# Kernel tuning notes

Measured on AMD Instinct MI355X. Metric: run time of the kernel, lower is better.

## Reference

```python
import jax, jax.numpy as jnp
import numpy as np

SHAPE = (4096, 8192)


def setup_inputs() -> dict:
    key = jax.random.key(0)
    k1, k2 = jax.random.split(key)
    weights = jax.random.normal(k1, SHAPE, dtype=jnp.float32)
    mask_weights = jax.random.normal(k2, SHAPE, dtype=jnp.float32)
    return {
        "weights": weights,
        "mask_weights": mask_weights,
        "masking_percent_x100": 50,
    }


def reference(weights, mask_weights, masking_percent_x100):
    # Faithful to MaskingFunction.forward:
    #   k = int((1 - masking_percent) * N); zero the k SMALLEST mask_weights positions in weights.
    masking_percent = masking_percent_x100 / 100.0
    n = mask_weights.size  # static
    k = int((1.0 - masking_percent) * n)  # static Python int -> jit-compatible
    flat_mask = mask_weights.reshape(-1)
    # bottom-k == top-k of negated values
    _, bottomk_idx = jax.lax.top_k(-flat_mask, k)
    masked = weights.reshape(-1).at[bottomk_idx].set(0.0)
    return masked.reshape(weights.shape)
```

## Files before the change

kernel.cpp:

```cpp
#include <hip/hip_runtime.h>


#define NBINS 2048
#define CAP1 (1u << 22)
#define CAP2 65536u

__device__ unsigned long long g_k;
__device__ long long          g_b1;
__device__ unsigned long long g_rem1;
__device__ unsigned int       g_hist1[NBINS];
__device__ unsigned int       g_hist2[NBINS];
__device__ unsigned int       g_count1;
__device__ unsigned int       g_count2;
__device__ unsigned long long g_kstar_excl;
__device__ unsigned int       g_cand_u[CAP1];
__device__ unsigned int       g_cand_i[CAP1];
__device__ unsigned long long g_cand2[CAP2];

static __device__ __forceinline__ unsigned int xf(unsigned int b) {
  return b ^ ((unsigned int)((int)b >> 31) | 0x80000000u);
}

__global__ __launch_bounds__(256) void k_init(const int* __restrict__ mp, long long n) {
  int t = threadIdx.x;
  for (int i = t; i < NBINS; i += 256) { g_hist1[i] = 0; g_hist2[i] = 0; }
  if (t == 0) {
    long long m = (long long)(*mp);
    long long k = (n * (100 - m)) / 100;
    if (k < 0) k = 0;
    if (k > n) k = n;
    g_k = (unsigned long long)k;
    g_count1 = 0;
    g_count2 = 0;
    g_kstar_excl = 0;
    g_b1 = -1;
    g_rem1 = 0;
  }
}

__global__ __launch_bounds__(256) void hist1_kernel(const unsigned int* __restrict__ mb,
                                                    long long n4, long long n) {
  __shared__ unsigned int sh[4 * NBINS];
  const int t = threadIdx.x;
  for (int i = t; i < 4 * NBINS; i += 256) sh[i] = 0;
  __syncthreads();
  unsigned int* h = &sh[(t >> 6) * NBINS];
  const long long stride = (long long)gridDim.x * 256;
  const uint4* mb4 = (const uint4*)mb;
  for (long long i = (long long)blockIdx.x * 256 + t; i < n4; i += stride) {
    uint4 v = mb4[i];
    atomicAdd(&h[xf(v.x) >> 21], 1u);
    atomicAdd(&h[xf(v.y) >> 21], 1u);
    atomicAdd(&h[xf(v.z) >> 21], 1u);
    atomicAdd(&h[xf(v.w) >> 21], 1u);
  }
  if (blockIdx.x == 0) {
    long long rs = n4 << 2;
    if ((long long)t < n - rs) atomicAdd(&h[xf(mb[rs + t]) >> 21], 1u);
  }
  __syncthreads();
  for (int i = t; i < NBINS; i += 256) {
    unsigned int s = sh[i] + sh[i + NBINS] + sh[i + 2 * NBINS] + sh[i + 3 * NBINS];
    if (s) atomicAdd(&g_hist1[i], s);
  }
}

__global__ __launch_bounds__(256) void select1_kernel() {
  __shared__ unsigned long long tsum[256];
  __shared__ long long s_bin;
  __shared__ unsigned long long s_rem;
  const int t = threadIdx.x;
  unsigned long long k = g_k;
  if (k == 0) return;
  unsigned int local[8];
  unsigned long long s = 0;
#pragma unroll
  for (int j = 0; j < 8; j++) { local[j] = g_hist1[t * 8 + j]; s += local[j]; }
  tsum[t] = s;
  __syncthreads();
  for (int off = 1; off < 256; off <<= 1) {
    unsigned long long v = (t >= off) ? tsum[t - off] : 0ull;
    __syncthreads();
    tsum[t] += v;
    __syncthreads();
  }
  unsigned long long incl = tsum[t], excl = incl - s;
  if (excl < k && k <= incl) {
    unsigned long long cum = excl;
#pragma unroll
    for (int j = 0; j < 8; j++) {
      if (cum + local[j] >= k) { s_bin = t * 8 + j; s_rem = k - cum; break; }
      cum += local[j];
    }
  }
  __syncthreads();
  if (t == 0) { g_b1 = s_bin; g_rem1 = s_rem; }
}

__global__ __launch_bounds__(256) void pass2_kernel(const unsigned int* __restrict__ mb,
                                                    const float* __restrict__ w,
                                                    float* __restrict__ out,
                                                    long long n4, long long n) {
  __shared__ unsigned int sh2[NBINS];
  const int t = threadIdx.x;
  for (int i = t; i < NBINS; i += 256) sh2[i] = 0;
  __syncthreads();
  const long long b1 = g_b1;
  const long long stride = (long long)gridDim.x * 256;
  const uint4*  mb4 = (const uint4*)mb;
  const float4* w4  = (const float4*)w;
  float4*       o4  = (float4*)out;
  for (long long i = (long long)blockIdx.x * 256 + t; i < n4; i += stride) {
    uint4  mv = mb4[i];
    float4 wv = w4[i];
    unsigned int u0 = xf(mv.x), u1 = xf(mv.y), u2 = xf(mv.z), u3 = xf(mv.w);
    float4 o;
    o.x = ((long long)(u0 >> 21) < b1) ? 0.0f : wv.x;
    o.y = ((long long)(u1 >> 21) < b1) ? 0.0f : wv.y;
    o.z = ((long long)(u2 >> 21) < b1) ? 0.0f : wv.z;
    o.w = ((long long)(u3 >> 21) < b1) ? 0.0f : wv.w;
    o4[i] = o;
    long long base = i << 2;
    if ((long long)(u0 >> 21) == b1) {
      unsigned int s = atomicAdd(&g_count1, 1u);
      if (s < CAP1) { g_cand_u[s] = u0; g_cand_i[s] = (unsigned int)(base + 0); }
      atomicAdd(&sh2[(u0 >> 10) & (NBINS - 1)], 1u);
    }
    if ((long long)(u1 >> 21) == b1) {
      unsigned int s = atomicAdd(&g_count1, 1u);
      if (s < CAP1) { g_cand_u[s] = u1; g_cand_i[s] = (unsigned int)(base + 1); }
      atomicAdd(&sh2[(u1 >> 10) & (NBINS - 1)], 1u);
    }
    if ((long long)(u2 >> 21) == b1) {
      unsigned int s = atomicAdd(&g_count1, 1u);
      if (s < CAP1) { g_cand_u[s] = u2; g_cand_i[s] = (unsigned int)(base + 2); }
      atomicAdd(&sh2[(u2 >> 10) & (NBINS - 1)], 1u);
    }
    if ((long long)(u3 >> 21) == b1) {
      unsigned int s = atomicAdd(&g_count1, 1u);
      if (s < CAP1) { g_cand_u[s] = u3; g_cand_i[s] = (unsigned int)(base + 3); }
      atomicAdd(&sh2[(u3 >> 10) & (NBINS - 1)], 1u);
    }
  }
  if (blockIdx.x == 0) {
    long long rs = n4 << 2;
    long long i = rs + t;
    if (i < n) {
      unsigned int u = xf(mb[i]);
      out[i] = ((long long)(u >> 21) < b1) ? 0.0f : w[i];
      if ((long long)(u >> 21) == b1) {
        unsigned int s = atomicAdd(&g_count1, 1u);
        if (s < CAP1) { g_cand_u[s] = u; g_cand_i[s] = (unsigned int)i; }
        atomicAdd(&sh2[(u >> 10) & (NBINS - 1)], 1u);
      }
    }
  }
  __syncthreads();
  for (int i = t; i < NBINS; i += 256)
    if (sh2[i]) atomicAdd(&g_hist2[i], sh2[i]);
}

__global__ __launch_bounds__(256) void finalize_kernel() {
  __shared__ unsigned long long tsum[256];
  __shared__ long long s_b2;
  __shared__ unsigned long long s_rem2;
  const int t = threadIdx.x;
  long long b1 = g_b1;
  if (b1 < 0) return;
  {
    unsigned long long k = g_rem1;
    unsigned int local[8];
    unsigned long long s = 0;
#pragma unroll
    for (int j = 0; j < 8; j++) { local[j] = g_hist2[t * 8 + j]; s += local[j]; }
    tsum[t] = s;
    __syncthreads();
    for (int off = 1; off < 256; off <<= 1) {
      unsigned long long v = (t >= off) ? tsum[t - off] : 0ull;
      __syncthreads();
      tsum[t] += v;
      __syncthreads();
    }
    unsigned long long incl = tsum[t], excl = incl - s;
    if (excl < k && k <= incl) {
      unsigned long long cum = excl;
#pragma unroll
      for (int j = 0; j < 8; j++) {
        if (cum + local[j] >= k) { s_b2 = t * 8 + j; s_rem2 = k - cum; break; }
        cum += local[j];
      }
    }
    __syncthreads();
  }
  const unsigned int b2 = (unsigned int)s_b2;
  const unsigned int C = (g_count1 < CAP1) ? g_count1 : CAP1;
  for (unsigned int i = t; i < C; i += 256) {
    unsigned int u = g_cand_u[i];
    if (((u >> 10) & (NBINS - 1)) == b2) {
      unsigned int slot = atomicAdd(&g_count2, 1u);
      if (slot < CAP2) g_cand2[slot] = ((unsigned long long)u << 32) | (unsigned long long)g_cand_i[i];
    }
  }
  __threadfence();
  __syncthreads();
  unsigned int c2 = atomicAdd(&g_count2, 0u);
  const unsigned int C2 = (c2 < CAP2) ? c2 : CAP2;
  const unsigned long long rem2 = s_rem2;
  for (unsigned int i = t; i < C2; i += 256) {
    unsigned long long key = g_cand2[i];
    unsigned long long cnt = 0;
    for (unsigned int j = 0; j < C2; j++) cnt += (g_cand2[j] < key) ? 1ull : 0ull;
    if (cnt + 1 == rem2) g_kstar_excl = key + 1;
  }
}

__global__ __launch_bounds__(256) void fixup_kernel(float* __restrict__ out) {
  const unsigned long long kstar = g_kstar_excl;
  const unsigned int C = (g_count1 < CAP1) ? g_count1 : CAP1;
  const long long stride = (long long)gridDim.x * blockDim.x;
  for (long long i = (long long)blockIdx.x * blockDim.x + threadIdx.x; i < (long long)C; i += stride) {
    unsigned int idx = g_cand_i[i];
    unsigned long long key = ((unsigned long long)g_cand_u[i] << 32) | (unsigned long long)idx;
    if (key < kstar) out[idx] = 0.0f;
  }
}

extern "C" void kernel_launch(void* const* d_in, const int* in_sizes, int n_in,
                              void* d_out, int out_size, void* d_ws, size_t ws_size,
                              hipStream_t stream) {
  const float*        w  = (const float*)d_in[0];
  const unsigned int* mb = (const unsigned int*)d_in[1];
  const int*          mp = (const int*)d_in[2];
  float* out = (float*)d_out;
  const long long n  = (long long)in_sizes[0];
  const long long n4 = n >> 2;

  int blocks = (int)((n4 + 255) / 256);
  if (blocks > 2048) blocks = 2048;
  if (blocks < 1) blocks = 1;

  k_init<<<1, 256, 0, stream>>>(mp, n);
  hist1_kernel<<<blocks, 256, 0, stream>>>(mb, n4, n);
  select1_kernel<<<1, 256, 0, stream>>>();
  pass2_kernel<<<blocks, 256, 0, stream>>>(mb, w, out, n4, n);
  finalize_kernel<<<1, 256, 0, stream>>>();
  fixup_kernel<<<256, 256, 0, stream>>>(out);
}
```

Measured before the change: 368.3 us.

## Fuse select/init/fixup stages into fewer kernels and unroll streaming loops

Cuts the pipeline from six launches to three. The bin-select prefix scan is folded into every pass2 block. The init kernel is replaced by resetting the histograms and counters at the end of finalize, and the fixup scatter now runs inside the single-block finalize. The hist1 loop is unrolled to four uint4 loads per thread and the pass2 loop to two. The pass2 second-level histogram now uses global atomics directly instead of a shared histogram. The aim is to remove launch overhead and add memory-level parallelism, at the cost of redundant per-block scans and reliance on globals starting at zero on the first call.

```diff
diff --git a/kernel.cpp b/kernel.cpp
--- a/kernel.cpp
+++ b/kernel.cpp
@@ -5,14 +5,10 @@
 #define CAP1 (1u << 22)
 #define CAP2 65536u
 
-__device__ unsigned long long g_k;
-__device__ long long          g_b1;
-__device__ unsigned long long g_rem1;
 __device__ unsigned int       g_hist1[NBINS];
 __device__ unsigned int       g_hist2[NBINS];
 __device__ unsigned int       g_count1;
 __device__ unsigned int       g_count2;
-__device__ unsigned long long g_kstar_excl;
 __device__ unsigned int       g_cand_u[CAP1];
 __device__ unsigned int       g_cand_i[CAP1];
 __device__ unsigned long long g_cand2[CAP2];
@@ -21,21 +17,12 @@
   return b ^ ((unsigned int)((int)b >> 31) | 0x80000000u);
 }
 
-__global__ __launch_bounds__(256) void k_init(const int* __restrict__ mp, long long n) {
-  int t = threadIdx.x;
-  for (int i = t; i < NBINS; i += 256) { g_hist1[i] = 0; g_hist2[i] = 0; }
-  if (t == 0) {
-    long long m = (long long)(*mp);
-    long long k = (n * (100 - m)) / 100;
-    if (k < 0) k = 0;
-    if (k > n) k = n;
-    g_k = (unsigned long long)k;
-    g_count1 = 0;
-    g_count2 = 0;
-    g_kstar_excl = 0;
-    g_b1 = -1;
-    g_rem1 = 0;
-  }
+static __device__ __forceinline__ long long compute_k(const int* mp, long long n) {
+  long long m = (long long)(*mp);
+  long long k = (n * (100 - m)) / 100;
+  if (k < 0) k = 0;
+  if (k > n) k = n;
+  return k;
 }
 
 __global__ __launch_bounds__(256) void hist1_kernel(const unsigned int* __restrict__ mb,
@@ -45,14 +32,40 @@
   for (int i = t; i < 4 * NBINS; i += 256) sh[i] = 0;
   __syncthreads();
   unsigned int* h = &sh[(t >> 6) * NBINS];
-  const long long stride = (long long)gridDim.x * 256;
   const uint4* mb4 = (const uint4*)mb;
-  for (long long i = (long long)blockIdx.x * 256 + t; i < n4; i += stride) {
-    uint4 v = mb4[i];
-    atomicAdd(&h[xf(v.x) >> 21], 1u);
-    atomicAdd(&h[xf(v.y) >> 21], 1u);
-    atomicAdd(&h[xf(v.z) >> 21], 1u);
-    atomicAdd(&h[xf(v.w) >> 21], 1u);
+  const long long stride = (long long)gridDim.x * 1024;
+  long long i0 = (long long)blockIdx.x * 1024 + t;
+  for (; i0 + 768 < n4; i0 += stride) {
+    uint4 v0 = mb4[i0];
+    uint4 v1 = mb4[i0 + 256];
+    uint4 v2 = mb4[i0 + 512];
+    uint4 v3 = mb4[i0 + 768];
+    atomicAdd(&h[xf(v0.x) >> 21], 1u);
+    atomicAdd(&h[xf(v0.y) >> 21], 1u);
+    atomicAdd(&h[xf(v0.z) >> 21], 1u);
+    atomicAdd(&h[xf(v0.w) >> 21], 1u);
+    atomicAdd(&h[xf(v1.x) >> 21], 1u);
+    atomicAdd(&h[xf(v1.y) >> 21], 1u);
+    atomicAdd(&h[xf(v1.z) >> 21], 1u);
+    atomicAdd(&h[xf(v1.w) >> 21], 1u);
+    atomicAdd(&h[xf(v2.x) >> 21], 1u);
+    atomicAdd(&h[xf(v2.y) >> 21], 1u);
+    atomicAdd(&h[xf(v2.z) >> 21], 1u);
+    atomicAdd(&h[xf(v2.w) >> 21], 1u);
+    atomicAdd(&h[xf(v3.x) >> 21], 1u);
+    atomicAdd(&h[xf(v3.y) >> 21], 1u);
+    atomicAdd(&h[xf(v3.z) >> 21], 1u);
+    atomicAdd(&h[xf(v3.w) >> 21], 1u);
+  }
+  for (int g = 0; g < 3; ++g) {
+    long long i = i0 + (long long)g * 256;
+    if (i < n4) {
+      uint4 v = mb4[i];
+      atomicAdd(&h[xf(v.x) >> 21], 1u);
+      atomicAdd(&h[xf(v.y) >> 21], 1u);
+      atomicAdd(&h[xf(v.z) >> 21], 1u);
+      atomicAdd(&h[xf(v.w) >> 21], 1u);
+    }
   }
   if (blockIdx.x == 0) {
     long long rs = n4 << 2;
@@ -65,82 +78,82 @@
   }
 }
 
-__global__ __launch_bounds__(256) void select1_kernel() {
-  __shared__ unsigned long long tsum[256];
-  __shared__ long long s_bin;
-  __shared__ unsigned long long s_rem;
-  const int t = threadIdx.x;
-  unsigned long long k = g_k;
-  if (k == 0) return;
-  unsigned int local[8];
-  unsigned long long s = 0;
-#pragma unroll
-  for (int j = 0; j < 8; j++) { local[j] = g_hist1[t * 8 + j]; s += local[j]; }
-  tsum[t] = s;
-  __syncthreads();
-  for (int off = 1; off < 256; off <<= 1) {
-    unsigned long long v = (t >= off) ? tsum[t - off] : 0ull;
-    __syncthreads();
-    tsum[t] += v;
-    __syncthreads();
-  }
-  unsigned long long incl = tsum[t], excl = incl - s;
-  if (excl < k && k <= incl) {
-    unsigned long long cum = excl;
-#pragma unroll
-    for (int j = 0; j < 8; j++) {
-      if (cum + local[j] >= k) { s_bin = t * 8 + j; s_rem = k - cum; break; }
-      cum += local[j];
-    }
-  }
-  __syncthreads();
-  if (t == 0) { g_b1 = s_bin; g_rem1 = s_rem; }
+static __device__ __forceinline__ void cand_add(unsigned int u, unsigned int idx) {
+  unsigned int s = atomicAdd(&g_count1, 1u);
+  if (s < CAP1) { g_cand_u[s] = u; g_cand_i[s] = idx; }
+  atomicAdd(&g_hist2[(u >> 10) & (NBINS - 1)], 1u);
+}
+
+static __device__ __forceinline__ void proc4(long long i, uint4 mv, float4 wv,
+                                             float4* __restrict__ o4, long long b1) {
+  unsigned int u0 = xf(mv.x), u1 = xf(mv.y), u2 = xf(mv.z), u3 = xf(mv.w);
+  float4 o;
+  o.x = ((long long)(u0 >> 21) < b1) ? 0.0f : wv.x;
+  o.y = ((long long)(u1 >> 21) < b1) ? 0.0f : wv.y;
+  o.z = ((long long)(u2 >> 21) < b1) ? 0.0f : wv.z;
+  o.w = ((long long)(u3 >> 21) < b1) ? 0.0f : wv.w;
+  o4[i] = o;
+  long long base = i << 2;
+  if ((long long)(u0 >> 21) == b1) cand_add(u0, (unsigned int)(base + 0));
+  if ((long long)(u1 >> 21) == b1) cand_add(u1, (unsigned int)(base + 1));
+  if ((long long)(u2 >> 21) == b1) cand_add(u2, (unsigned int)(base + 2));
+  if ((long long)(u3 >> 21) == b1) cand_add(u3, (unsigned int)(base + 3));
 }
 
 __global__ __launch_bounds__(256) void pass2_kernel(const unsigned int* __restrict__ mb,
                                                     const float* __restrict__ w,
                                                     float* __restrict__ out,
+                                                    const int* __restrict__ mp,
                                                     long long n4, long long n) {
-  __shared__ unsigned int sh2[NBINS];
+  __shared__ unsigned long long tsum[256];
+  __shared__ long long s_b1;
   const int t = threadIdx.x;
-  for (int i = t; i < NBINS; i += 256) sh2[i] = 0;
-  __syncthreads();
-  const long long b1 = g_b1;
-  const long long stride = (long long)gridDim.x * 256;
+  if (t == 0) s_b1 = -1;
+  __syncthreads();
+  const unsigned long long k = (unsigned long long)compute_k(mp, n);
+  if (k != 0) {
+    unsigned int local[8];
+    unsigned long long s = 0;
+#pragma unroll
+    for (int j = 0; j < 8; j++) { local[j] = g_hist1[t * 8 + j]; s += local[j]; }
+    tsum[t] = s;
+    __syncthreads();
+    for (int off = 1; off < 256; off <<= 1) {
+      unsigned long long v = (t >= off) ? tsum[t - off] : 0ull;
+      __syncthreads();
+      tsum[t] += v;
+      __syncthreads();
+    }
+    unsigned long long incl = tsum[t], excl = incl - s;
+    if (excl < k && k <= incl) {
+      unsigned long long cum = excl;
+#pragma unroll
+      for (int j = 0; j < 8; j++) {
+        if (cum + local[j] >= k) { s_b1 = t * 8 + j; break; }
+        cum += local[j];
+      }
+    }
+  }
+  __syncthreads();
+  const long long b1 = s_b1;
+
   const uint4*  mb4 = (const uint4*)mb;
   const float4* w4  = (const float4*)w;
   float4*       o4  = (float4*)out;
-  for (long long i = (long long)blockIdx.x * 256 + t; i < n4; i += stride) {
-    uint4  mv = mb4[i];
-    float4 wv = w4[i];
-    unsigned int u0 = xf(mv.x), u1 = xf(mv.y), u2 = xf(mv.z), u3 = xf(mv.w);
-    float4 o;
-    o.x = ((long long)(u0 >> 21) < b1) ? 0.0f : wv.x;
-    o.y = ((long long)(u1 >> 21) < b1) ? 0.0f : wv.y;
-    o.z = ((long long)(u2 >> 21) < b1) ? 0.0f : wv.z;
-    o.w = ((long long)(u3 >> 21) < b1) ? 0.0f : wv.w;
-    o4[i] = o;
-    long long base = i << 2;
-    if ((long long)(u0 >> 21) == b1) {
-      unsigned int s = atomicAdd(&g_count1, 1u);
-      if (s < CAP1) { g_cand_u[s] = u0; g_cand_i[s] = (unsigned int)(base + 0); }
-      atomicAdd(&sh2[(u0 >> 10) & (NBINS - 1)], 1u);
-    }
-    if ((long long)(u1 >> 21) == b1) {
-      unsigned int s = atomicAdd(&g_count1, 1u);
-      if (s < CAP1) { g_cand_u[s] = u1; g_cand_i[s] = (unsigned int)(base + 1); }
-      atomicAdd(&sh2[(u1 >> 10) & (NBINS - 1)], 1u);
-    }
-    if ((long long)(u2 >> 21) == b1) {
-      unsigned int s = atomicAdd(&g_count1, 1u);
-      if (s < CAP1) { g_cand_u[s] = u2; g_cand_i[s] = (unsigned int)(base + 2); }
-      atomicAdd(&sh2[(u2 >> 10) & (NBINS - 1)], 1u);
-    }
-    if ((long long)(u3 >> 21) == b1) {
-      unsigned int s = atomicAdd(&g_count1, 1u);
-      if (s < CAP1) { g_cand_u[s] = u3; g_cand_i[s] = (unsigned int)(base + 3); }
-      atomicAdd(&sh2[(u3 >> 10) & (NBINS - 1)], 1u);
-    }
+  const long long stride = (long long)gridDim.x * 512;
+  long long i0 = (long long)blockIdx.x * 512 + t;
+  for (; i0 + 256 < n4; i0 += stride) {
+    uint4  mv0 = mb4[i0];
+    uint4  mv1 = mb4[i0 + 256];
+    float4 wv0 = w4[i0];
+    float4 wv1 = w4[i0 + 256];
+    proc4(i0, mv0, wv0, o4, b1);
+    proc4(i0 + 256, mv1, wv1, o4, b1);
+  }
+  if (i0 < n4) {
+    uint4  mv = mb4[i0];
+    float4 wv = w4[i0];
+    proc4(i0, mv, wv, o4, b1);
   }
   if (blockIdx.x == 0) {
     long long rs = n4 << 2;
@@ -148,81 +161,102 @@
     if (i < n) {
       unsigned int u = xf(mb[i]);
       out[i] = ((long long)(u >> 21) < b1) ? 0.0f : w[i];
-      if ((long long)(u >> 21) == b1) {
-        unsigned int s = atomicAdd(&g_count1, 1u);
-        if (s < CAP1) { g_cand_u[s] = u; g_cand_i[s] = (unsigned int)i; }
-        atomicAdd(&sh2[(u >> 10) & (NBINS - 1)], 1u);
-      }
-    }
-  }
-  __syncthreads();
-  for (int i = t; i < NBINS; i += 256)
-    if (sh2[i]) atomicAdd(&g_hist2[i], sh2[i]);
-}
-
-__global__ __launch_bounds__(256) void finalize_kernel() {
+      if ((long long)(u >> 21) == b1) cand_add(u, (unsigned int)i);
+    }
+  }
+}
+
+__global__ __launch_bounds__(256) void finalize_kernel(const int* __restrict__ mp,
+                                                       float* __restrict__ out,
+                                                       long long n) {
   __shared__ unsigned long long tsum[256];
   __shared__ long long s_b2;
-  __shared__ unsigned long long s_rem2;
+  __shared__ unsigned long long s_rem1, s_rem2, s_kstar;
   const int t = threadIdx.x;
-  long long b1 = g_b1;
-  if (b1 < 0) return;
-  {
-    unsigned long long k = g_rem1;
-    unsigned int local[8];
-    unsigned long long s = 0;
-#pragma unroll
-    for (int j = 0; j < 8; j++) { local[j] = g_hist2[t * 8 + j]; s += local[j]; }
-    tsum[t] = s;
+  const unsigned long long k = (unsigned long long)compute_k(mp, n);
+  if (k != 0) {
+    if (t == 0) s_kstar = 0;
+    {
+      unsigned int local[8];
+      unsigned long long s = 0;
+#pragma unroll
+      for (int j = 0; j < 8; j++) { local[j] = g_hist1[t * 8 + j]; s += local[j]; }
+      tsum[t] = s;
+      __syncthreads();
+      for (int off = 1; off < 256; off <<= 1) {
+        unsigned long long v = (t >= off) ? tsum[t - off] : 0ull;
+        __syncthreads();
+        tsum[t] += v;
+        __syncthreads();
+      }
+      unsigned long long incl = tsum[t], excl = incl - s;
+      if (excl < k && k <= incl) {
+        unsigned long long cum = excl;
+#pragma unroll
+        for (int j = 0; j < 8; j++) {
+          if (cum + local[j] >= k) { s_rem1 = k - cum; break; }
+          cum += local[j];
+        }
+      }
+      __syncthreads();
+    }
+    {
+      unsigned long long k2 = s_rem1;
+      __syncthreads();
+      unsigned int local[8];
+      unsigned long long s = 0;
+#pragma unroll
+      for (int j = 0; j < 8; j++) { local[j] = g_hist2[t * 8 + j]; s += local[j]; }
+      tsum[t] = s;
+      __syncthreads();
+      for (int off = 1; off < 256; off <<= 1) {
+        unsigned long long v = (t >= off) ? tsum[t - off] : 0ull;
+        __syncthreads();
+        tsum[t] += v;
+        __syncthreads();
+      }
+      unsigned long long incl = tsum[t], excl = incl - s;
+      if (excl < k2 && k2 <= incl) {
+        unsigned long long cum = excl;
+#pragma unroll
+        for (int j = 0; j < 8; j++) {
+          if (cum + local[j] >= k2) { s_b2 = t * 8 + j; s_rem2 = k2 - cum; break; }
+          cum += local[j];
+        }
+      }
+      __syncthreads();
+    }
+    const unsigned int b2 = (unsigned int)s_b2;
+    const unsigned int C = (g_count1 < CAP1) ? g_count1 : CAP1;
+    for (unsigned int i = t; i < C; i += 256) {
+      unsigned int u = g_cand_u[i];
+      if (((u >> 10) & (NBINS - 1)) == b2) {
+        unsigned int slot = atomicAdd(&g_count2, 1u);
+        if (slot < CAP2) g_cand2[slot] = ((unsigned long long)u << 32) | (unsigned long long)g_cand_i[i];
+      }
+    }
+    __threadfence();
     __syncthreads();
-    for (int off = 1; off < 256; off <<= 1) {
-      unsigned long long v = (t >= off) ? tsum[t - off] : 0ull;
-      __syncthreads();
-      tsum[t] += v;
-      __syncthreads();
-    }
-    unsigned long long incl = tsum[t], excl = incl - s;
-    if (excl < k && k <= incl) {
-      unsigned long long cum = excl;
-#pragma unroll
-      for (int j = 0; j < 8; j++) {
-        if (cum + local[j] >= k) { s_b2 = t * 8 + j; s_rem2 = k - cum; break; }
-        cum += local[j];
-      }
+    unsigned int c2 = atomicAdd(&g_count2, 0u);
+    const unsigned int C2 = (c2 < CAP2) ? c2 : CAP2;
+    const unsigned long long rem2 = s_rem2;
+    for (unsigned int i = t; i < C2; i += 256) {
+      unsigned long long key = g_cand2[i];
+      unsigned long long cnt = 0;
+      for (unsigned int j = 0; j < C2; j++) cnt += (g_cand2[j] < key) ? 1ull : 0ull;
+      if (cnt + 1 == rem2) s_kstar = key + 1;
     }
     __syncthreads();
-  }
-  const unsigned int b2 = (unsigned int)s_b2;
-  const unsigned int C = (g_count1 < CAP1) ? g_count1 : CAP1;
-  for (unsigned int i = t; i < C; i += 256) {
-    unsigned int u = g_cand_u[i];
-    if (((u >> 10) & (NBINS - 1)) == b2) {
-      unsigned int slot = atomicAdd(&g_count2, 1u);
-      if (slot < CAP2) g_cand2[slot] = ((unsigned long long)u << 32) | (unsigned long long)g_cand_i[i];
-    }
-  }
-  __threadfence();
-  __syncthreads();
-  unsigned int c2 = atomicAdd(&g_count2, 0u);
-  const unsigned int C2 = (c2 < CAP2) ? c2 : CAP2;
-  const unsigned long long rem2 = s_rem2;
-  for (unsigned int i = t; i < C2; i += 256) {
-    unsigned long long key = g_cand2[i];
-    unsigned long long cnt = 0;
-    for (unsigned int j = 0; j < C2; j++) cnt += (g_cand2[j] < key) ? 1ull : 0ull;
-    if (cnt + 1 == rem2) g_kstar_excl = key + 1;
-  }
-}
-
-__global__ __launch_bounds__(256) void fixup_kernel(float* __restrict__ out) {
-  const unsigned long long kstar = g_kstar_excl;
-  const unsigned int C = (g_count1 < CAP1) ? g_count1 : CAP1;
-  const long long stride = (long long)gridDim.x * blockDim.x;
-  for (long long i = (long long)blockIdx.x * blockDim.x + threadIdx.x; i < (long long)C; i += stride) {
-    unsigned int idx = g_cand_i[i];
-    unsigned long long key = ((unsigned long long)g_cand_u[i] << 32) | (unsigned long long)idx;
-    if (key < kstar) out[idx] = 0.0f;
-  }
+    const unsigned long long kstar = s_kstar;
+    for (unsigned int i = t; i < C; i += 256) {
+      unsigned int idx = g_cand_i[i];
+      unsigned long long key = ((unsigned long long)g_cand_u[i] << 32) | (unsigned long long)idx;
+      if (key < kstar) out[idx] = 0.0f;
+    }
+  }
+  __syncthreads();
+  for (int i = t; i < NBINS; i += 256) { g_hist1[i] = 0; g_hist2[i] = 0; }
+  if (t == 0) { g_count1 = 0; g_count2 = 0; }
 }
 
 extern "C" void kernel_launch(void* const* d_in, const int* in_sizes, int n_in,
@@ -235,14 +269,14 @@
   const long long n  = (long long)in_sizes[0];
   const long long n4 = n >> 2;
 
-  int blocks = (int)((n4 + 255) / 256);
-  if (blocks > 2048) blocks = 2048;
-  if (blocks < 1) blocks = 1;
-
-  k_init<<<1, 256, 0, stream>>>(mp, n);
-  hist1_kernel<<<blocks, 256, 0, stream>>>(mb, n4, n);
-  select1_kernel<<<1, 256, 0, stream>>>();
-  pass2_kernel<<<blocks, 256, 0, stream>>>(mb, w, out, n4, n);
-  finalize_kernel<<<1, 256, 0, stream>>>();
-  fixup_kernel<<<256, 256, 0, stream>>>(out);
-}
+  long long g1 = (n4 + 1023) / 1024;
+  if (g1 < 1) g1 = 1;
+  if (g1 > 1024) g1 = 1024;
+  long long g2 = (n4 + 511) / 512;
+  if (g2 < 1) g2 = 1;
+  if (g2 > 2048) g2 = 2048;
+
+  hist1_kernel<<<(int)g1, 256, 0, stream>>>(mb, n4, n);
+  pass2_kernel<<<(int)g2, 256, 0, stream>>>(mb, w, out, mp, n4, n);
+  finalize_kernel<<<1, 256, 0, stream>>>(mp, out, n);
+}
```

Result: faster. 354.1 us (-3.9%).
